# Optimization experiments

Hardware: AMD Instinct MI355X
Metric: run time of the kernel (lower is better)

## Reference

```python
import jax, jax.numpy as jnp
import numpy as np

GROUP_SIZE = 128


def setup_inputs() -> dict:
    key = jax.random.key(0)
    k1, k2, k3 = jax.random.split(key, 3)
    B, S, IN, OUT = 4, 8192, 1024, 1024
    x = jax.random.normal(k1, (B, S, IN), dtype=jnp.float32)
    weight = jax.random.normal(k2, (OUT, IN), dtype=jnp.float32) * 0.02
    bias = jax.random.normal(k3, (OUT,), dtype=jnp.float32) * 0.01
    return {"x": x, "weight": weight, "bias": bias}


def reference(x, weight, bias):
    """Quantized int8 path: quantize() + _forward_int8 of OneBitLinear.

    - weights binarized to +/-1 int8 (sign, with 0 -> -1, matching
      sign().clamp(min=0) bit packing then 2*bit-1)
    - per-group weight scales = group absmax, stored fp16 (as in quantize())
    - activations dynamically quantized per-token to int8
    - int32-accumulated GEMM, rescaled by x_scale * mean group scale per row
    """
    out_f, in_f = weight.shape
    ng = in_f // GROUP_SIZE
    w_g = weight.reshape(out_f, ng, GROUP_SIZE)
    # per-group absmax scales, cast fp16 -> fp32 to mimic fp16 storage
    scales = jnp.maximum(jnp.max(jnp.abs(w_g), axis=-1), 1e-8)
    scales = scales.astype(jnp.float16).astype(jnp.float32)  # [O, ng]
    # +/-1 int8 weights (sign>0 -> +1, else -1; zero maps to -1 like the packer)
    w_int8 = jnp.where(weight > 0, 1, -1).astype(jnp.int8)  # [O, I]

    # dynamic per-token activation quantization
    x_f = x.reshape(-1, in_f)  # [BT, I]
    x_scale = jnp.maximum(jnp.max(jnp.abs(x_f), axis=1, keepdims=True), 1e-8) / 127.0
    x_int8 = jnp.clip(jnp.round(x_f / x_scale), -128, 127).astype(jnp.int8)

    # int8 GEMM with int32 accumulation
    out_i32 = jnp.matmul(
        x_int8.astype(jnp.int32), w_int8.T.astype(jnp.int32)
    )  # [BT, O]

    w_scale_per_row = jnp.mean(scales, axis=1)  # [O]
    out_f32 = out_i32.astype(jnp.float32) * x_scale * w_scale_per_row[None, :]
    out_f32 = out_f32 + bias[None, :]
    return out_f32.reshape(*x.shape[:-1], out_f)
```

## Files before the change

kernel.cpp:

```cpp
#include <hip/hip_runtime.h>
#include <hip/hip_fp16.h>

#define K_DIM 1024
#define N_DIM 1024

typedef int v4i __attribute__((ext_vector_type(4)));

__device__ __forceinline__ void async_load16(const void* g, void* l) {
    __builtin_amdgcn_global_load_lds(
        (const __attribute__((address_space(1))) unsigned int*)g,
        (__attribute__((address_space(3))) unsigned int*)l,
        16, 0, 0);
}

__global__ __launch_bounds__(256) void prep_w(const float* __restrict__ w,
                                              signed char* __restrict__ wq,
                                              float* __restrict__ wscale) {
    const int lane = threadIdx.x & 63;
    const int row  = blockIdx.x * 4 + (threadIdx.x >> 6);
    const float4* wr = (const float4*)(w + (size_t)row * K_DIM);
    float4 v[4];
#pragma unroll
    for (int j = 0; j < 4; ++j) v[j] = wr[lane * 4 + j];

    float g = 0.f;
#pragma unroll
    for (int j = 0; j < 4; ++j) {
        g = fmaxf(g, fabsf(v[j].x)); g = fmaxf(g, fabsf(v[j].y));
        g = fmaxf(g, fabsf(v[j].z)); g = fmaxf(g, fabsf(v[j].w));
    }
    g = fmaxf(g, __shfl_xor(g, 1, 64));
    g = fmaxf(g, __shfl_xor(g, 2, 64));
    g = fmaxf(g, __shfl_xor(g, 4, 64));
    const float s = __half2float(__float2half(fmaxf(g, 1e-8f)));
    float t = s;
    t += __shfl_xor(t, 8, 64);
    t += __shfl_xor(t, 16, 64);
    t += __shfl_xor(t, 32, 64);
    if (lane == 0) wscale[row] = t * 0.125f;

    int pk[4];
#pragma unroll
    for (int j = 0; j < 4; ++j) {
        const int b0 = (v[j].x > 0.f) ? 1 : -1;
        const int b1 = (v[j].y > 0.f) ? 1 : -1;
        const int b2 = (v[j].z > 0.f) ? 1 : -1;
        const int b3 = (v[j].w > 0.f) ? 1 : -1;
        pk[j] = (b0 & 255) | ((b1 & 255) << 8) | ((b2 & 255) << 16) | (b3 << 24);
    }
    *(int4*)(wq + (size_t)row * K_DIM + lane * 16) = make_int4(pk[0], pk[1], pk[2], pk[3]);
}

__global__ __launch_bounds__(256) void quant_x(const float* __restrict__ x,
                                               signed char* __restrict__ xq,
                                               float* __restrict__ xs) {
    const int lane = threadIdx.x & 63;
    const int row  = blockIdx.x * 4 + (threadIdx.x >> 6);
    const float4* xr = (const float4*)(x + (size_t)row * K_DIM);
    float4 v[4];
#pragma unroll
    for (int j = 0; j < 4; ++j) v[j] = xr[lane * 4 + j];

    float am = 0.f;
#pragma unroll
    for (int j = 0; j < 4; ++j) {
        am = fmaxf(am, fabsf(v[j].x)); am = fmaxf(am, fabsf(v[j].y));
        am = fmaxf(am, fabsf(v[j].z)); am = fmaxf(am, fabsf(v[j].w));
    }
#pragma unroll
    for (int off = 32; off >= 1; off >>= 1) am = fmaxf(am, __shfl_xor(am, off, 64));
    const float scale = fmaxf(am, 1e-8f) / 127.f;
    const float inv   = 1.0f / scale;

    int pk[4];
#pragma unroll
    for (int j = 0; j < 4; ++j) {
        const int b0 = (int)fminf(fmaxf(rintf(v[j].x * inv), -128.f), 127.f);
        const int b1 = (int)fminf(fmaxf(rintf(v[j].y * inv), -128.f), 127.f);
        const int b2 = (int)fminf(fmaxf(rintf(v[j].z * inv), -128.f), 127.f);
        const int b3 = (int)fminf(fmaxf(rintf(v[j].w * inv), -128.f), 127.f);
        pk[j] = (b0 & 255) | ((b1 & 255) << 8) | ((b2 & 255) << 16) | (b3 << 24);
    }
    *(int4*)(xq + (size_t)row * K_DIM + lane * 16) = make_int4(pk[0], pk[1], pk[2], pk[3]);
    if (lane == 0) xs[row] = scale;
}

__global__ __launch_bounds__(256) void gemm_i8(const signed char* __restrict__ A,
                                               const signed char* __restrict__ Bw,
                                               const float* __restrict__ xs,
                                               const float* __restrict__ wscale,
                                               const float* __restrict__ bias,
                                               float* __restrict__ out) {
    __shared__ __align__(16) signed char As[128 * 128];
    __shared__ __align__(16) signed char Bs[128 * 128];

    const int tid  = threadIdx.x;
    const int lane = tid & 63;
    const int wave = tid >> 6;
    const int wm = wave >> 1;
    const int wn = wave & 1;

    const int bid = blockIdx.x;
    const int xcd = bid & 7;
    const int q   = bid >> 3;
    const int mT  = xcd * 32 + (q >> 3);
    const int nT  = q & 7;
    const size_t mBase = (size_t)mT * 128;
    const int    nBase = nT * 128;

    v4i acc[4][4] = {};

    const int srow = tid >> 3;
    const int scol = (((tid & 7) ^ (srow & 7))) * 16;
    const signed char* Ag = A  + (mBase + srow) * K_DIM + scol;
    const signed char* Bg = Bw + (size_t)(nBase + srow) * K_DIM + scol;

    for (int kt = 0; kt < 8; ++kt) {
        const int koff = kt * 128;
#pragma unroll
        for (int c = 0; c < 4; ++c) {
            async_load16(Ag + (size_t)(c * 32) * K_DIM + koff, As + c * 4096 + tid * 16);
            async_load16(Bg + (size_t)(c * 32) * K_DIM + koff, Bs + c * 4096 + tid * 16);
        }
        __syncthreads();

        const int r16 = lane & 15;
        const int g   = lane >> 4;
        const int x7  = lane & 7;
#pragma unroll
        for (int ks = 0; ks < 2; ++ks) {
            const int co = ((ks * 4 + g) ^ x7) * 16;
            v4i af[4], bf[4];
#pragma unroll
            for (int mt = 0; mt < 4; ++mt)
                af[mt] = *(const v4i*)(As + (wm * 64 + mt * 16 + r16) * 128 + co);
#pragma unroll
            for (int nt = 0; nt < 4; ++nt)
                bf[nt] = *(const v4i*)(Bs + (wn * 64 + nt * 16 + r16) * 128 + co);
#pragma unroll
            for (int mt = 0; mt < 4; ++mt)
#pragma unroll
                for (int nt = 0; nt < 4; ++nt)
                    acc[mt][nt] = __builtin_amdgcn_mfma_i32_16x16x64_i8(
                        af[mt], bf[nt], acc[mt][nt], 0, 0, 0);
        }
        __syncthreads();
    }

    const int cc = lane & 15;
    const int rq = (lane >> 4) * 4;
    float xsr[4][4];
#pragma unroll
    for (int mt = 0; mt < 4; ++mt)
#pragma unroll
        for (int i = 0; i < 4; ++i)
            xsr[mt][i] = xs[mBase + wm * 64 + mt * 16 + rq + i];

#pragma unroll
    for (int nt = 0; nt < 4; ++nt) {
        const int col  = nBase + wn * 64 + nt * 16 + cc;
        const float wsc = wscale[col];
        const float bb  = bias[col];
#pragma unroll
        for (int mt = 0; mt < 4; ++mt) {
#pragma unroll
            for (int i = 0; i < 4; ++i) {
                const size_t row = mBase + wm * 64 + mt * 16 + rq + i;
                out[row * N_DIM + col] = ((float)acc[mt][nt][i] * xsr[mt][i]) * wsc + bb;
            }
        }
    }
}

extern "C" void kernel_launch(void* const* d_in, const int* in_sizes, int n_in,
                              void* d_out, int out_size, void* d_ws, size_t ws_size,
                              hipStream_t stream) {
    const float* x    = (const float*)d_in[0];
    const float* w    = (const float*)d_in[1];
    const float* bias = (const float*)d_in[2];
    float* out = (float*)d_out;

    const int BT = in_sizes[0] / K_DIM;

    char* ws = (char*)d_ws;
    signed char* xq     = (signed char*)ws;
    float*       xs     = (float*)(ws + (size_t)BT * K_DIM);
    signed char* wq     = (signed char*)(ws + (size_t)BT * K_DIM + (size_t)BT * 4);
    float*       wscale = (float*)((char*)wq + (size_t)N_DIM * K_DIM);

    prep_w<<<N_DIM / 4, 256, 0, stream>>>(w, wq, wscale);
    quant_x<<<BT / 4, 256, 0, stream>>>(x, xq, xs);
    gemm_i8<<<(BT / 128) * (N_DIM / 128), 256, 0, stream>>>(xq, wq, xs, wscale, bias, out);
}
```

Baseline: 276.5 us.

## Enlarge GEMM tiles to 256x256 with double-buffered async LDS pipeline

```diff
diff --git a/kernel.cpp b/kernel.cpp
--- a/kernel.cpp
+++ b/kernel.cpp
@@ -12,6 +12,11 @@
         (__attribute__((address_space(3))) unsigned int*)l,
         16, 0, 0);
 }
+
+#define BAR() do { asm volatile("" ::: "memory"); \
+                   __builtin_amdgcn_s_barrier();  \
+                   asm volatile("" ::: "memory"); } while (0)
+#define VMCNT0() asm volatile("s_waitcnt vmcnt(0)" ::: "memory")
 
 __global__ __launch_bounds__(256) void prep_w(const float* __restrict__ w,
                                               signed char* __restrict__ wq,
@@ -85,88 +90,102 @@
     if (lane == 0) xs[row] = scale;
 }
 
-__global__ __launch_bounds__(256) void gemm_i8(const signed char* __restrict__ A,
-                                               const signed char* __restrict__ Bw,
-                                               const float* __restrict__ xs,
-                                               const float* __restrict__ wscale,
-                                               const float* __restrict__ bias,
-                                               float* __restrict__ out) {
-    __shared__ __align__(16) signed char As[128 * 128];
-    __shared__ __align__(16) signed char Bs[128 * 128];
+__global__ __launch_bounds__(512, 2) void gemm_i8(const signed char* __restrict__ A,
+                                                  const signed char* __restrict__ Bw,
+                                                  const float* __restrict__ xs,
+                                                  const float* __restrict__ wscale,
+                                                  const float* __restrict__ bias,
+                                                  float* __restrict__ out) {
+    __shared__ __align__(16) signed char As[2][256 * 64];
+    __shared__ __align__(16) signed char Bs[2][256 * 64];
 
     const int tid  = threadIdx.x;
     const int lane = tid & 63;
     const int wave = tid >> 6;
-    const int wm = wave >> 1;
-    const int wn = wave & 1;
-
-    const int bid = blockIdx.x;
-    const int xcd = bid & 7;
-    const int q   = bid >> 3;
-    const int mT  = xcd * 32 + (q >> 3);
-    const int nT  = q & 7;
-    const size_t mBase = (size_t)mT * 128;
-    const int    nBase = nT * 128;
-
-    v4i acc[4][4] = {};
-
-    const int srow = tid >> 3;
-    const int scol = (((tid & 7) ^ (srow & 7))) * 16;
-    const signed char* Ag = A  + (mBase + srow) * K_DIM + scol;
-    const signed char* Bg = Bw + (size_t)(nBase + srow) * K_DIM + scol;
-
-    for (int kt = 0; kt < 8; ++kt) {
-        const int koff = kt * 128;
-#pragma unroll
-        for (int c = 0; c < 4; ++c) {
-            async_load16(Ag + (size_t)(c * 32) * K_DIM + koff, As + c * 4096 + tid * 16);
-            async_load16(Bg + (size_t)(c * 32) * K_DIM + koff, Bs + c * 4096 + tid * 16);
+    const int wm   = wave >> 2;
+    const int wn   = wave & 3;
+
+    const int bid  = blockIdx.x;
+    const int wgid = (bid & 7) * 64 + (bid >> 3);
+    const int mT   = wgid >> 2;
+    const int nT   = wgid & 3;
+    const size_t mBase = (size_t)mT * 256;
+    const int    nBase = nT * 256;
+
+    const int srow = tid >> 2;
+    const int skq  = (tid & 3) * 16;
+    const signed char* Ag = A  + (mBase + srow) * K_DIM + skq;
+    const signed char* Bg = Bw + (size_t)(nBase + srow) * K_DIM + skq;
+    const int soff = tid * 16;
+
+#define STAGE(b, kt) do {                                                   \
+        const int _ko = (kt) * 64;                                          \
+        async_load16(Ag + _ko,                         &As[b][soff]);       \
+        async_load16(Ag + (size_t)128 * K_DIM + _ko,   &As[b][8192 + soff]);\
+        async_load16(Bg + _ko,                         &Bs[b][soff]);       \
+        async_load16(Bg + (size_t)128 * K_DIM + _ko,   &Bs[b][8192 + soff]);\
+    } while (0)
+
+    v4i acc[8][4] = {};
+
+    const int r16 = lane & 15;
+    const int g16 = (lane >> 4) * 16;
+    const int aoff = (wm * 128 + r16) * 64 + g16;
+    const int boff = (wn * 64  + r16) * 64 + g16;
+
+    STAGE(0, 0);
+    VMCNT0();
+    BAR();
+
+    for (int t = 0; t < 16; ++t) {
+        const signed char* Ab = As[t & 1];
+        const signed char* Bb = Bs[t & 1];
+
+        if (t < 15) STAGE((t + 1) & 1, t + 1);
+
+        v4i af[8], bf[4];
+#pragma unroll
+        for (int mf = 0; mf < 8; ++mf)
+            af[mf] = *(const v4i*)(Ab + aoff + mf * (16 * 64));
+#pragma unroll
+        for (int nf = 0; nf < 4; ++nf)
+            bf[nf] = *(const v4i*)(Bb + boff + nf * (16 * 64));
+
+#pragma unroll
+        for (int mf = 0; mf < 8; ++mf)
+#pragma unroll
+            for (int nf = 0; nf < 4; ++nf)
+                acc[mf][nf] = __builtin_amdgcn_mfma_i32_16x16x64_i8(
+                    af[mf], bf[nf], acc[mf][nf], 0, 0, 0);
+
+        if (t < 15) {
+            __builtin_amdgcn_sched_barrier(0);
+            VMCNT0();
+            BAR();
         }
-        __syncthreads();
-
-        const int r16 = lane & 15;
-        const int g   = lane >> 4;
-        const int x7  = lane & 7;
-#pragma unroll
-        for (int ks = 0; ks < 2; ++ks) {
-            const int co = ((ks * 4 + g) ^ x7) * 16;
-            v4i af[4], bf[4];
-#pragma unroll
-            for (int mt = 0; mt < 4; ++mt)
-                af[mt] = *(const v4i*)(As + (wm * 64 + mt * 16 + r16) * 128 + co);
-#pragma unroll
-            for (int nt = 0; nt < 4; ++nt)
-                bf[nt] = *(const v4i*)(Bs + (wn * 64 + nt * 16 + r16) * 128 + co);
-#pragma unroll
-            for (int mt = 0; mt < 4; ++mt)
-#pragma unroll
-                for (int nt = 0; nt < 4; ++nt)
-                    acc[mt][nt] = __builtin_amdgcn_mfma_i32_16x16x64_i8(
-                        af[mt], bf[nt], acc[mt][nt], 0, 0, 0);
-        }
-        __syncthreads();
-    }
-
-    const int cc = lane & 15;
+    }
+#undef STAGE
+
+    const int cc = r16;
     const int rq = (lane >> 4) * 4;
-    float xsr[4][4];
-#pragma unroll
-    for (int mt = 0; mt < 4; ++mt)
+    float xsr[8][4];
+#pragma unroll
+    for (int mf = 0; mf < 8; ++mf)
 #pragma unroll
         for (int i = 0; i < 4; ++i)
-            xsr[mt][i] = xs[mBase + wm * 64 + mt * 16 + rq + i];
-
-#pragma unroll
-    for (int nt = 0; nt < 4; ++nt) {
-        const int col  = nBase + wn * 64 + nt * 16 + cc;
+            xsr[mf][i] = xs[mBase + wm * 128 + mf * 16 + rq + i];
+
+#pragma unroll
+    for (int nf = 0; nf < 4; ++nf) {
+        const int col  = nBase + wn * 64 + nf * 16 + cc;
         const float wsc = wscale[col];
         const float bb  = bias[col];
 #pragma unroll
-        for (int mt = 0; mt < 4; ++mt) {
+        for (int mf = 0; mf < 8; ++mf) {
 #pragma unroll
             for (int i = 0; i < 4; ++i) {
-                const size_t row = mBase + wm * 64 + mt * 16 + rq + i;
-                out[row * N_DIM + col] = ((float)acc[mt][nt][i] * xsr[mt][i]) * wsc + bb;
+                const size_t row = mBase + wm * 128 + mf * 16 + rq + i;
+                out[row * N_DIM + col] = (float)acc[mf][nf][i] * xsr[mf][i] * wsc + bb;
             }
         }
     }
@@ -190,5 +209,5 @@
 
     prep_w<<<N_DIM / 4, 256, 0, stream>>>(w, wq, wscale);
     quant_x<<<BT / 4, 256, 0, stream>>>(x, xq, xs);
-    gemm_i8<<<(BT / 128) * (N_DIM / 128), 256, 0, stream>>>(xq, wq, xs, wscale, bias, out);
-}
+    gemm_i8<<<(BT / 256) * (N_DIM / 256), 512, 0, stream>>>(xq, wq, xs, wscale, bias, out);
+}
```

After: 303.5 us. 9.8% more time.

## Triple-buffer GEMM K-loop with async LDS loads and merge prep kernels

Applied to the files above, without the earlier changes.

```diff
diff --git a/kernel.cpp b/kernel.cpp
--- a/kernel.cpp
+++ b/kernel.cpp
@@ -13,86 +13,90 @@
         16, 0, 0);
 }
 
-__global__ __launch_bounds__(256) void prep_w(const float* __restrict__ w,
-                                              signed char* __restrict__ wq,
-                                              float* __restrict__ wscale) {
+#define BAR() do { asm volatile("" ::: "memory"); \
+                   __builtin_amdgcn_s_barrier();  \
+                   asm volatile("" ::: "memory"); } while (0)
+
+__global__ __launch_bounds__(256) void prep_quant(const float* __restrict__ w,
+                                                  const float* __restrict__ x,
+                                                  signed char* __restrict__ wq,
+                                                  float* __restrict__ wscale,
+                                                  signed char* __restrict__ xq,
+                                                  float* __restrict__ xs) {
     const int lane = threadIdx.x & 63;
-    const int row  = blockIdx.x * 4 + (threadIdx.x >> 6);
-    const float4* wr = (const float4*)(w + (size_t)row * K_DIM);
-    float4 v[4];
-#pragma unroll
-    for (int j = 0; j < 4; ++j) v[j] = wr[lane * 4 + j];
-
-    float g = 0.f;
-#pragma unroll
-    for (int j = 0; j < 4; ++j) {
-        g = fmaxf(g, fabsf(v[j].x)); g = fmaxf(g, fabsf(v[j].y));
-        g = fmaxf(g, fabsf(v[j].z)); g = fmaxf(g, fabsf(v[j].w));
+    if (blockIdx.x < 256) {
+        const int row = blockIdx.x * 4 + (threadIdx.x >> 6);
+        const float4* wr = (const float4*)(w + (size_t)row * K_DIM);
+        float4 v[4];
+#pragma unroll
+        for (int j = 0; j < 4; ++j) v[j] = wr[lane * 4 + j];
+
+        float g = 0.f;
+#pragma unroll
+        for (int j = 0; j < 4; ++j) {
+            g = fmaxf(g, fabsf(v[j].x)); g = fmaxf(g, fabsf(v[j].y));
+            g = fmaxf(g, fabsf(v[j].z)); g = fmaxf(g, fabsf(v[j].w));
+        }
+        g = fmaxf(g, __shfl_xor(g, 1, 64));
+        g = fmaxf(g, __shfl_xor(g, 2, 64));
+        g = fmaxf(g, __shfl_xor(g, 4, 64));
+        const float s = __half2float(__float2half(fmaxf(g, 1e-8f)));
+        float t = s;
+        t += __shfl_xor(t, 8, 64);
+        t += __shfl_xor(t, 16, 64);
+        t += __shfl_xor(t, 32, 64);
+        if (lane == 0) wscale[row] = t * 0.125f;
+
+        int pk[4];
+#pragma unroll
+        for (int j = 0; j < 4; ++j) {
+            const int b0 = (v[j].x > 0.f) ? 1 : -1;
+            const int b1 = (v[j].y > 0.f) ? 1 : -1;
+            const int b2 = (v[j].z > 0.f) ? 1 : -1;
+            const int b3 = (v[j].w > 0.f) ? 1 : -1;
+            pk[j] = (b0 & 255) | ((b1 & 255) << 8) | ((b2 & 255) << 16) | (b3 << 24);
+        }
+        *(int4*)(wq + (size_t)row * K_DIM + lane * 16) = make_int4(pk[0], pk[1], pk[2], pk[3]);
+    } else {
+        const int row = (blockIdx.x - 256) * 4 + (threadIdx.x >> 6);
+        const float4* xr = (const float4*)(x + (size_t)row * K_DIM);
+        float4 v[4];
+#pragma unroll
+        for (int j = 0; j < 4; ++j) v[j] = xr[lane * 4 + j];
+
+        float am = 0.f;
+#pragma unroll
+        for (int j = 0; j < 4; ++j) {
+            am = fmaxf(am, fabsf(v[j].x)); am = fmaxf(am, fabsf(v[j].y));
+            am = fmaxf(am, fabsf(v[j].z)); am = fmaxf(am, fabsf(v[j].w));
+        }
+#pragma unroll
+        for (int off = 32; off >= 1; off >>= 1) am = fmaxf(am, __shfl_xor(am, off, 64));
+        const float scale = fmaxf(am, 1e-8f) / 127.f;
+        const float inv   = 1.0f / scale;
+
+        int pk[4];
+#pragma unroll
+        for (int j = 0; j < 4; ++j) {
+            const int b0 = (int)fminf(fmaxf(rintf(v[j].x * inv), -128.f), 127.f);
+            const int b1 = (int)fminf(fmaxf(rintf(v[j].y * inv), -128.f), 127.f);
+            const int b2 = (int)fminf(fmaxf(rintf(v[j].z * inv), -128.f), 127.f);
+            const int b3 = (int)fminf(fmaxf(rintf(v[j].w * inv), -128.f), 127.f);
+            pk[j] = (b0 & 255) | ((b1 & 255) << 8) | ((b2 & 255) << 16) | (b3 << 24);
+        }
+        *(int4*)(xq + (size_t)row * K_DIM + lane * 16) = make_int4(pk[0], pk[1], pk[2], pk[3]);
+        if (lane == 0) xs[row] = scale;
     }
-    g = fmaxf(g, __shfl_xor(g, 1, 64));
-    g = fmaxf(g, __shfl_xor(g, 2, 64));
-    g = fmaxf(g, __shfl_xor(g, 4, 64));
-    const float s = __half2float(__float2half(fmaxf(g, 1e-8f)));
-    float t = s;
-    t += __shfl_xor(t, 8, 64);
-    t += __shfl_xor(t, 16, 64);
-    t += __shfl_xor(t, 32, 64);
-    if (lane == 0) wscale[row] = t * 0.125f;
-
-    int pk[4];
-#pragma unroll
-    for (int j = 0; j < 4; ++j) {
-        const int b0 = (v[j].x > 0.f) ? 1 : -1;
-        const int b1 = (v[j].y > 0.f) ? 1 : -1;
-        const int b2 = (v[j].z > 0.f) ? 1 : -1;
-        const int b3 = (v[j].w > 0.f) ? 1 : -1;
-        pk[j] = (b0 & 255) | ((b1 & 255) << 8) | ((b2 & 255) << 16) | (b3 << 24);
-    }
-    *(int4*)(wq + (size_t)row * K_DIM + lane * 16) = make_int4(pk[0], pk[1], pk[2], pk[3]);
-}
-
-__global__ __launch_bounds__(256) void quant_x(const float* __restrict__ x,
-                                               signed char* __restrict__ xq,
-                                               float* __restrict__ xs) {
-    const int lane = threadIdx.x & 63;
-    const int row  = blockIdx.x * 4 + (threadIdx.x >> 6);
-    const float4* xr = (const float4*)(x + (size_t)row * K_DIM);
-    float4 v[4];
-#pragma unroll
-    for (int j = 0; j < 4; ++j) v[j] = xr[lane * 4 + j];
-
-    float am = 0.f;
-#pragma unroll
-    for (int j = 0; j < 4; ++j) {
-        am = fmaxf(am, fabsf(v[j].x)); am = fmaxf(am, fabsf(v[j].y));
-        am = fmaxf(am, fabsf(v[j].z)); am = fmaxf(am, fabsf(v[j].w));
-    }
-#pragma unroll
-    for (int off = 32; off >= 1; off >>= 1) am = fmaxf(am, __shfl_xor(am, off, 64));
-    const float scale = fmaxf(am, 1e-8f) / 127.f;
-    const float inv   = 1.0f / scale;
-
-    int pk[4];
-#pragma unroll
-    for (int j = 0; j < 4; ++j) {
-        const int b0 = (int)fminf(fmaxf(rintf(v[j].x * inv), -128.f), 127.f);
-        const int b1 = (int)fminf(fmaxf(rintf(v[j].y * inv), -128.f), 127.f);
-        const int b2 = (int)fminf(fmaxf(rintf(v[j].z * inv), -128.f), 127.f);
-        const int b3 = (int)fminf(fmaxf(rintf(v[j].w * inv), -128.f), 127.f);
-        pk[j] = (b0 & 255) | ((b1 & 255) << 8) | ((b2 & 255) << 16) | (b3 << 24);
-    }
-    *(int4*)(xq + (size_t)row * K_DIM + lane * 16) = make_int4(pk[0], pk[1], pk[2], pk[3]);
-    if (lane == 0) xs[row] = scale;
-}
-
-__global__ __launch_bounds__(256) void gemm_i8(const signed char* __restrict__ A,
-                                               const signed char* __restrict__ Bw,
-                                               const float* __restrict__ xs,
-                                               const float* __restrict__ wscale,
-                                               const float* __restrict__ bias,
-                                               float* __restrict__ out) {
-    __shared__ __align__(16) signed char As[128 * 128];
-    __shared__ __align__(16) signed char Bs[128 * 128];
+}
+
+__global__ __launch_bounds__(256, 3) void gemm_i8(const signed char* __restrict__ A,
+                                                  const signed char* __restrict__ Bw,
+                                                  const float* __restrict__ xs,
+                                                  const float* __restrict__ wscale,
+                                                  const float* __restrict__ bias,
+                                                  float* __restrict__ out) {
+    __shared__ __align__(16) signed char As[3][128 * 64];
+    __shared__ __align__(16) signed char Bs[3][128 * 64];
 
     const int tid  = threadIdx.x;
     const int lane = tid & 63;
@@ -108,65 +112,76 @@
     const size_t mBase = (size_t)mT * 128;
     const int    nBase = nT * 128;
 
-    v4i acc[4][4] = {};
-
-    const int srow = tid >> 3;
-    const int scol = (((tid & 7) ^ (srow & 7))) * 16;
+    const int srow = tid >> 2;
+    const int scol = ((tid & 3) ^ (srow & 3)) * 16;
+    const int soff = tid * 16;
     const signed char* Ag = A  + (mBase + srow) * K_DIM + scol;
     const signed char* Bg = Bw + (size_t)(nBase + srow) * K_DIM + scol;
 
-    for (int kt = 0; kt < 8; ++kt) {
-        const int koff = kt * 128;
-#pragma unroll
-        for (int c = 0; c < 4; ++c) {
-            async_load16(Ag + (size_t)(c * 32) * K_DIM + koff, As + c * 4096 + tid * 16);
-            async_load16(Bg + (size_t)(c * 32) * K_DIM + koff, Bs + c * 4096 + tid * 16);
-        }
-        __syncthreads();
-
-        const int r16 = lane & 15;
-        const int g   = lane >> 4;
-        const int x7  = lane & 7;
-#pragma unroll
-        for (int ks = 0; ks < 2; ++ks) {
-            const int co = ((ks * 4 + g) ^ x7) * 16;
-            v4i af[4], bf[4];
-#pragma unroll
-            for (int mt = 0; mt < 4; ++mt)
-                af[mt] = *(const v4i*)(As + (wm * 64 + mt * 16 + r16) * 128 + co);
-#pragma unroll
-            for (int nt = 0; nt < 4; ++nt)
-                bf[nt] = *(const v4i*)(Bs + (wn * 64 + nt * 16 + r16) * 128 + co);
-#pragma unroll
-            for (int mt = 0; mt < 4; ++mt)
-#pragma unroll
-                for (int nt = 0; nt < 4; ++nt)
-                    acc[mt][nt] = __builtin_amdgcn_mfma_i32_16x16x64_i8(
-                        af[mt], bf[nt], acc[mt][nt], 0, 0, 0);
-        }
-        __syncthreads();
+#define STAGE(b, kt) do {                                                \
+        const int _ko = (kt) * 64;                                       \
+        async_load16(Ag + _ko,                      As[b] + soff);       \
+        async_load16(Ag + (size_t)64 * K_DIM + _ko, As[b] + 4096 + soff);\
+        async_load16(Bg + _ko,                      Bs[b] + soff);       \
+        async_load16(Bg + (size_t)64 * K_DIM + _ko, Bs[b] + 4096 + soff);\
+    } while (0)
+
+    v4i acc[4][4] = {};
+    const int r16 = lane & 15;
+    const int g   = lane >> 4;
+    const int co  = (g ^ (r16 & 3)) * 16;
+
+    STAGE(0, 0);
+    STAGE(1, 1);
+
+    for (int t = 0; t < 16; ++t) {
+        if (t == 15) asm volatile("s_waitcnt vmcnt(0)" ::: "memory");
+        else         asm volatile("s_waitcnt vmcnt(4)" ::: "memory");
+        BAR();
+        if (t < 14) STAGE((t + 2) % 3, t + 2);
+
+        const signed char* Ab = As[t % 3];
+        const signed char* Bb = Bs[t % 3];
+        v4i af[4], bf[4];
+#pragma unroll
+        for (int mf = 0; mf < 4; ++mf)
+            af[mf] = *(const v4i*)(Ab + ((wm * 64 + mf * 16 + r16) << 6) + co);
+#pragma unroll
+        for (int nf = 0; nf < 4; ++nf)
+            bf[nf] = *(const v4i*)(Bb + ((wn * 64 + nf * 16 + r16) << 6) + co);
+
+#pragma unroll
+        for (int mf = 0; mf < 4; ++mf)
+#pragma unroll
+            for (int nf = 0; nf < 4; ++nf)
+                acc[mf][nf] = __builtin_amdgcn_mfma_i32_16x16x64_i8(
+                    af[mf], bf[nf], acc[mf][nf], 0, 0, 0);
+
+        __builtin_amdgcn_sched_barrier(0);
+        asm volatile("s_waitcnt lgkmcnt(0)" ::: "memory");
     }
-
-    const int cc = lane & 15;
+#undef STAGE
+
+    const int cc = r16;
     const int rq = (lane >> 4) * 4;
     float xsr[4][4];
 #pragma unroll
-    for (int mt = 0; mt < 4; ++mt)
+    for (int mf = 0; mf < 4; ++mf)
 #pragma unroll
         for (int i = 0; i < 4; ++i)
-            xsr[mt][i] = xs[mBase + wm * 64 + mt * 16 + rq + i];
-
-#pragma unroll
-    for (int nt = 0; nt < 4; ++nt) {
-        const int col  = nBase + wn * 64 + nt * 16 + cc;
+            xsr[mf][i] = xs[mBase + wm * 64 + mf * 16 + rq + i];
+
+#pragma unroll
+    for (int nf = 0; nf < 4; ++nf) {
+        const int col   = nBase + wn * 64 + nf * 16 + cc;
         const float wsc = wscale[col];
         const float bb  = bias[col];
 #pragma unroll
-        for (int mt = 0; mt < 4; ++mt) {
+        for (int mf = 0; mf < 4; ++mf) {
 #pragma unroll
             for (int i = 0; i < 4; ++i) {
-                const size_t row = mBase + wm * 64 + mt * 16 + rq + i;
-                out[row * N_DIM + col] = ((float)acc[mt][nt][i] * xsr[mt][i]) * wsc + bb;
+                const size_t row = mBase + wm * 64 + mf * 16 + rq + i;
+                out[row * N_DIM + col] = (float)acc[mf][nf][i] * xsr[mf][i] * wsc + bb;
             }
         }
     }
@@ -188,7 +203,6 @@
     signed char* wq     = (signed char*)(ws + (size_t)BT * K_DIM + (size_t)BT * 4);
     float*       wscale = (float*)((char*)wq + (size_t)N_DIM * K_DIM);
 
-    prep_w<<<N_DIM / 4, 256, 0, stream>>>(w, wq, wscale);
-    quant_x<<<BT / 4, 256, 0, stream>>>(x, xq, xs);
+    prep_quant<<<256 + BT / 4, 256, 0, stream>>>(w, x, wq, wscale, xq, xs);
     gemm_i8<<<(BT / 128) * (N_DIM / 128), 256, 0, stream>>>(xq, wq, xs, wscale, bias, out);
 }
```

Measured after the change: 271.9 us. No clear change (-1.7%).
